# Optimization experiments

Hardware: AMD Instinct MI355X
Metric: run time of the kernel (lower is better)

The kernel has to match this reference:

```python
import jax, jax.numpy as jnp
import numpy as np

N, E, R = 50000, 800000, 8
EMB, PROJ, H, OUT = 512, 256, 256, 200


def rgcn_conv(x, src, dst, rel, W, root, bias):
    # PyG RGCNConv: per-relation linear transform, mean aggregation per relation
    # over incoming edges, summed across relations, plus root transform + bias.
    n = x.shape[0]
    r, _, out_dim = W.shape
    h = jnp.einsum('ni,rio->nro', x, W)            # [N,R,out] per-relation transforms
    msgs = h[src, rel]                             # [E,out] gather per-edge messages
    seg = dst * r + rel                            # combined (node, relation) segment id
    sums = jax.ops.segment_sum(msgs, seg, num_segments=n * r)
    cnt = jax.ops.segment_sum(jnp.ones((src.shape[0],), x.dtype), seg, num_segments=n * r)
    mean = sums / jnp.maximum(cnt, 1.0)[:, None]
    agg = mean.reshape(n, r, out_dim).sum(axis=1)  # sum over relations
    return agg + x @ root + bias


def setup_inputs() -> dict:
    key = jax.random.key(0)
    ks = jax.random.split(key, 16)
    inp = {
        'embeddings': jax.random.normal(ks[0], (N, EMB), jnp.float32),
        'node_indices': jnp.arange(N, dtype=jnp.int64) if jax.config.jax_enable_x64 else jnp.arange(N, dtype=jnp.int32),
        'src': jax.random.randint(ks[1], (E,), 0, N),
        'dst': jax.random.randint(ks[2], (E,), 0, N),
        'rel': jax.random.randint(ks[3], (E,), 0, R),
        'neg_src': jax.random.randint(ks[4], (E,), 0, N),
        'neg_dst': jax.random.randint(ks[5], (E,), 0, N),
        'neg_rel': jax.random.randint(ks[6], (E,), 0, R),
        # learned parameters
        'Wp': jax.random.normal(ks[7], (EMB, PROJ), jnp.float32) * 0.04,
        'bp': jnp.zeros((PROJ,), jnp.float32),
        'W0': jax.random.normal(ks[8], (R, PROJ, H), jnp.float32) * 0.06,
        'root0': jax.random.normal(ks[9], (PROJ, H), jnp.float32) * 0.06,
        'b0': jnp.zeros((H,), jnp.float32),
        'W1': jax.random.normal(ks[10], (R, H, H), jnp.float32) * 0.06,
        'root1': jax.random.normal(ks[11], (H, H), jnp.float32) * 0.06,
        'b1': jnp.zeros((H,), jnp.float32),
        'W2': jax.random.normal(ks[12], (R, H, OUT), jnp.float32) * 0.06,
        'root2': jax.random.normal(ks[13], (H, OUT), jnp.float32) * 0.06,
        'b2': jnp.zeros((OUT,), jnp.float32),
        'rel_emb': jax.random.normal(ks[14], (R, OUT), jnp.float32),
    }
    return inp


def reference(embeddings, node_indices, src, dst, rel, neg_src, neg_dst, neg_rel,
              Wp, bp, W0, root0, b0, W1, root1, b1, W2, root2, b2, rel_emb):
    # projection: Linear per modality, then reorder rows by node index (sort)
    proj = embeddings @ Wp + bp                        # [N,PROJ]
    x = jnp.zeros_like(proj).at[node_indices].set(proj)
    # stacked RGCN encoder with relu between layers (no relu on last)
    x = jax.nn.relu(rgcn_conv(x, src, dst, rel, W0, root0, b0))
    x = jax.nn.relu(rgcn_conv(x, src, dst, rel, W1, root1, b1))
    out = rgcn_conv(x, src, dst, rel, W2, root2, b2)   # [N,OUT]
    # DistMult decoder over positive + negative triples
    s = jnp.concatenate([src, neg_src])
    o = jnp.concatenate([dst, neg_dst])
    r = jnp.concatenate([rel, neg_rel])
    scores = jnp.sum(out[s] * rel_emb[r] * out[o], axis=-1)  # [2E]
    return out, scores
```

## Files before the change

### kernel.cpp

```cpp
#include <hip/hip_runtime.h>
#include <stdint.h>

#define NN 50000
#define NE 800000
#define NR 8
#define EMBD 512
#define PROJD 256
#define HIDD 256
#define OUTD 200
#define NSEG (NN * NR)
#define CSR_CAP 1536

typedef _Float16 half8 __attribute__((ext_vector_type(8)));
typedef _Float16 half4 __attribute__((ext_vector_type(4)));
typedef float f32x4 __attribute__((ext_vector_type(4)));

__device__ __forceinline__ void gload16(const void* g, void* l) {
    __builtin_amdgcn_global_load_lds(
        reinterpret_cast<const __attribute__((address_space(1))) uint32_t*>(
            reinterpret_cast<uintptr_t>(g)),
        reinterpret_cast<__attribute__((address_space(3))) uint32_t*>(
            reinterpret_cast<uintptr_t>(l)),
        16, 0, 0);
}


__global__ void count_edges(const int* __restrict__ dst, const int* __restrict__ rel,
                            int* __restrict__ cnt, int E) {
    int e = blockIdx.x * 256 + threadIdx.x;
    if (e >= E) return;
    atomicAdd(&cnt[dst[e] * NR + rel[e]], 1);
}

__global__ __launch_bounds__(512) void scan1(const int* __restrict__ cnt, int* __restrict__ offs,
                                             int* __restrict__ bsums, int n) {
    __shared__ int sm[512];
    int tid = threadIdx.x;
    int g = blockIdx.x * 512 + tid;
    int v = (g < n) ? cnt[g] : 0;
    sm[tid] = v;
    __syncthreads();
    for (int o = 1; o < 512; o <<= 1) {
        int t = (tid >= o) ? sm[tid - o] : 0;
        __syncthreads();
        sm[tid] += t;
        __syncthreads();
    }
    if (g < n) offs[g] = sm[tid] - v;
    if (tid == 511) bsums[blockIdx.x] = sm[511];
}

__global__ __launch_bounds__(1024) void scan2(const int* __restrict__ bsums, int* __restrict__ bpref, int nb) {
    __shared__ int sm[1024];
    int tid = threadIdx.x;
    int v = (tid < nb) ? bsums[tid] : 0;
    sm[tid] = v;
    __syncthreads();
    for (int o = 1; o < 1024; o <<= 1) {
        int t = (tid >= o) ? sm[tid - o] : 0;
        __syncthreads();
        sm[tid] += t;
        __syncthreads();
    }
    if (tid < nb) bpref[tid] = sm[tid] - v;
}

__global__ __launch_bounds__(512) void scan3(int* __restrict__ offs, int* __restrict__ cursor,
                                             const int* __restrict__ bpref, int n, int total) {
    int g = blockIdx.x * 512 + threadIdx.x;
    if (g < n) {
        int v = offs[g] + bpref[blockIdx.x];
        offs[g] = v;
        cursor[g] = v;
    }
    if (g == 0) offs[n] = total;
}

__global__ void pad_offs(int* __restrict__ offs, int total) {
    offs[NSEG + 1 + blockIdx.x * 256 + threadIdx.x] = total;
}

__global__ void scatter_edges(const int* __restrict__ dst, const int* __restrict__ rel,
                              const int* __restrict__ src, int* __restrict__ cursor,
                              int* __restrict__ csr, int E) {
    int e = blockIdx.x * 256 + threadIdx.x;
    if (e >= E) return;
    int seg = dst[e] * NR + rel[e];
    int pos = atomicAdd(&cursor[seg], 1);
    csr[pos] = src[e];
}


__global__ void f32_to_f16_vec(const float* __restrict__ in, _Float16* __restrict__ out, long n4) {
    long i = (long)blockIdx.x * 256 + threadIdx.x;
    long stride = (long)gridDim.x * 256;
    for (; i < n4; i += stride) {
        float4 v = ((const float4*)in)[i];
        half4 h;
        h[0] = (_Float16)v.x; h[1] = (_Float16)v.y; h[2] = (_Float16)v.z; h[3] = (_Float16)v.w;
        ((half4*)out)[i] = h;
    }
}

__global__ void build_bt(const float* __restrict__ S0, int K0, const float* __restrict__ S1,
                         _Float16* __restrict__ Bt, int N, int K) {
    int k = blockIdx.x * 256 + threadIdx.x;
    int n = blockIdx.y;
    if (k >= K) return;
    float v = (k < K0) ? S0[(size_t)k * N + n] : S1[(size_t)(k - K0) * N + n];
    Bt[(size_t)n * K + k] = (_Float16)v;
}


template <bool RELU, bool LAST>
__global__ __launch_bounds__(512, 4) void rgcn_layer(
    const _Float16* __restrict__ x, const _Float16* __restrict__ Bt,
    const int* __restrict__ csr, const int* __restrict__ offs,
    const float* __restrict__ bias,
    _Float16* __restrict__ C16, int ldc, float* __restrict__ C32, int N) {
    __shared__ _Float16 As[64 * 256];
    __shared__ _Float16 Bs[2][256 * 32];
    __shared__ int offs_lds[520];
    __shared__ int csr_lds[CSR_CAP];
    const int tid = threadIdx.x;
    const int lane = tid & 63, wave = tid >> 6;
    const int lane32 = tid & 31, hw = tid >> 5;
    const int half_base = lane & 32;
    const int l15 = lane & 15, q = lane >> 4;
    const int wm = wave >> 2, wn = wave & 3;
    const int m0 = blockIdx.x * 64;
    const int segbase = m0 * NR;

    for (int i = tid; i < 513; i += 512) offs_lds[i] = offs[segbase + i];
    __syncthreads();
    const int e0 = offs_lds[0];
    const int e1 = offs_lds[512];
    const int ecnt = min(e1 - e0, CSR_CAP);
    for (int i = tid; i < ecnt; i += 512) csr_lds[i] = csr[e0 + i];
    __syncthreads();

    auto stage = [&](int buf, int g) {
        int kbase = g * 32;
#pragma unroll
        for (int h = 0; h < 2; ++h) {
            int s = tid + h * 512;
            int n = s >> 2, c4 = s & 3;
            int nn = n < N ? n : N - 1;
            gload16(Bt + (size_t)nn * 2304 + kbase + ((c4 ^ (n & 3)) << 3),
                    &Bs[buf][(size_t)(wave * 64 + h * 512) * 8]);
        }
    };

    f32x4 acc[2][4] = {};
    stage(0, 0);
    int cur = 0;
    for (int seg = 0; seg < 9; ++seg) {
#pragma unroll
        for (int u = 0; u < 4; ++u) {
            int lr = u * 16 + hw;
            int nd = m0 + lr;
            if (nd >= NN) nd = NN - 1;
            half8 hv;
            if (seg == 0) {
                hv = *(const half8*)(x + (size_t)nd * 256 + lane32 * 8);
            } else {
                int sb = lr * NR + seg - 1;
                int o0 = offs_lds[sb], o1 = offs_lds[sb + 1];
                int n = o1 - o0;
                if (n < 0) n = 0;
                if (n == 0) {
#pragma unroll
                    for (int z = 0; z < 8; ++z) hv[z] = (_Float16)0.f;
                } else {
                    bool staged = (o1 - e0) <= CSR_CAP;
                    int fi = o0 + (lane32 < n ? lane32 : n - 1);
                    int idxv = staged ? csr_lds[fi - e0] : csr[fi];
                    float a0=0.f,a1=0.f,a2=0.f,a3=0.f,a4=0.f,a5=0.f,a6=0.f,a7=0.f;
                    int nb = n < 32 ? n : 32;
                    for (int e = 0; e < nb; e += 2) {
                        int s0 = __shfl(idxv, half_base + e);
                        half8 v0 = *(const half8*)(x + (size_t)s0 * 256 + lane32 * 8);
                        if (e + 1 < nb) {
                            int s1 = __shfl(idxv, half_base + e + 1);
                            half8 v1 = *(const half8*)(x + (size_t)s1 * 256 + lane32 * 8);
                            a0 += (float)v0[0] + (float)v1[0];
                            a1 += (float)v0[1] + (float)v1[1];
                            a2 += (float)v0[2] + (float)v1[2];
                            a3 += (float)v0[3] + (float)v1[3];
                            a4 += (float)v0[4] + (float)v1[4];
                            a5 += (float)v0[5] + (float)v1[5];
                            a6 += (float)v0[6] + (float)v1[6];
                            a7 += (float)v0[7] + (float)v1[7];
                        } else {
                            a0 += (float)v0[0]; a1 += (float)v0[1];
                            a2 += (float)v0[2]; a3 += (float)v0[3];
                            a4 += (float)v0[4]; a5 += (float)v0[5];
                            a6 += (float)v0[6]; a7 += (float)v0[7];
                        }
                    }
                    for (int e = 32; e < n; ++e) {
                        int s2 = staged ? csr_lds[o0 - e0 + e] : csr[o0 + e];
                        half8 v = *(const half8*)(x + (size_t)s2 * 256 + lane32 * 8);
                        a0 += (float)v[0]; a1 += (float)v[1];
                        a2 += (float)v[2]; a3 += (float)v[3];
                        a4 += (float)v[4]; a5 += (float)v[5];
                        a6 += (float)v[6]; a7 += (float)v[7];
                    }
                    float inv = 1.0f / (float)n;
                    hv[0] = (_Float16)(a0 * inv); hv[1] = (_Float16)(a1 * inv);
                    hv[2] = (_Float16)(a2 * inv); hv[3] = (_Float16)(a3 * inv);
                    hv[4] = (_Float16)(a4 * inv); hv[5] = (_Float16)(a5 * inv);
                    hv[6] = (_Float16)(a6 * inv); hv[7] = (_Float16)(a7 * inv);
                }
            }
            *(half8*)((char*)As + lr * 512 + ((lane32 ^ (lr & 31)) << 4)) = hv;
        }
        asm volatile("s_waitcnt lgkmcnt(0)" ::: "memory");
        __builtin_amdgcn_s_barrier();
        asm volatile("" ::: "memory");
        for (int ch = 0; ch < 8; ++ch) {
            int g = seg * 8 + ch;
            if (g < 71) {
                stage(cur ^ 1, g + 1);
                asm volatile("s_waitcnt vmcnt(2)" ::: "memory");
            } else {
                asm volatile("s_waitcnt vmcnt(0)" ::: "memory");
            }
            __builtin_amdgcn_s_barrier();
            asm volatile("" ::: "memory");
            half8 a[2], b[4];
#pragma unroll
            for (int i = 0; i < 2; ++i) {
                int row = wm * 32 + i * 16 + l15;
                int ck = ch * 4 + q;
                a[i] = *(const half8*)((const char*)As + row * 512 + ((ck ^ (row & 31)) << 4));
            }
#pragma unroll
            for (int j = 0; j < 4; ++j) {
                int n = wn * 64 + j * 16 + l15;
                b[j] = *(const half8*)((const char*)&Bs[cur][0] + n * 64 + ((q ^ (n & 3)) << 4));
            }
#pragma unroll
            for (int i = 0; i < 2; ++i)
#pragma unroll
                for (int j = 0; j < 4; ++j)
                    acc[i][j] = __builtin_amdgcn_mfma_f32_16x16x32_f16(a[i], b[j], acc[i][j], 0, 0, 0);
            asm volatile("s_waitcnt lgkmcnt(0)" ::: "memory");
            __builtin_amdgcn_s_barrier();
            asm volatile("" ::: "memory");
            cur ^= 1;
        }
    }
#pragma unroll
    for (int i = 0; i < 2; ++i) {
        int rbase = m0 + wm * 32 + i * 16 + q * 4;
#pragma unroll
        for (int j = 0; j < 4; ++j) {
            int cc = wn * 64 + j * 16 + l15;
            if (cc >= N) continue;
            float bv = bias[cc];
#pragma unroll
            for (int t = 0; t < 4; ++t) {
                int rr = rbase + t;
                if (rr >= NN) continue;
                float v = acc[i][j][t] + bv;
                if (RELU) v = fmaxf(v, 0.f);
                C16[(size_t)rr * ldc + cc] = (_Float16)v;
                if (LAST) C32[(size_t)rr * ldc + cc] = v;
            }
        }
    }
}


template <bool BIAS, bool ACC_IN, bool FINAL, bool RELU, bool LAST, bool SCATTER>
__global__ __launch_bounds__(256) void gemm16(
    const _Float16* __restrict__ A, int lda,
    const _Float16* __restrict__ Bt, int ldb,
    const float* __restrict__ bias, const int* __restrict__ sidx,
    _Float16* __restrict__ Cacc,
    _Float16* __restrict__ C16, int ldc, float* __restrict__ C32,
    int M, int N, int K) {
    __shared__ _Float16 As[2][4096];
    __shared__ _Float16 Bs[2][4096];
    const int tid = threadIdx.x;
    const int lane = tid & 63, wave = tid >> 6;
    const int wm = wave >> 1, wn = wave & 1;
    const int q = lane >> 4, l15 = lane & 15;
    const int m0 = blockIdx.y * 128, n0 = blockIdx.x * 128;
    const int wbase = wave * 512;
    f32x4 acc[4][4] = {};

    auto stage = [&](int buf, int k0) {
#pragma unroll
        for (int h = 0; h < 2; ++h) {
            int s = tid + h * 256;
            int r = s >> 2, c = s & 3;
            int cs = c ^ ((r >> 2) & 3);
            int ga = m0 + r; if (ga >= M) ga = M - 1;
            gload16(A + (size_t)ga * lda + k0 + cs * 8, &As[buf][wbase + h * 2048]);
            int gb = n0 + r; if (gb >= N) gb = N - 1;
            gload16(Bt + (size_t)gb * ldb + k0 + cs * 8, &Bs[buf][wbase + h * 2048]);
        }
    };

    const int nk = K >> 5;
    stage(0, 0);
    int cur = 0;
    for (int kt = 0; kt < nk; ++kt) {
        if (kt + 1 < nk) {
            stage(cur ^ 1, (kt + 1) << 5);
            asm volatile("s_waitcnt vmcnt(4)" ::: "memory");
        } else {
            asm volatile("s_waitcnt vmcnt(0)" ::: "memory");
        }
        __builtin_amdgcn_s_barrier();
        asm volatile("" ::: "memory");
        half8 a[4], b[4];
#pragma unroll
        for (int i = 0; i < 4; ++i) {
            int row = wm * 64 + i * 16 + l15;
            a[i] = *(const half8*)&As[cur][row * 32 + ((q ^ ((row >> 2) & 3)) << 3)];
            int col = wn * 64 + i * 16 + l15;
            b[i] = *(const half8*)&Bs[cur][col * 32 + ((q ^ ((col >> 2) & 3)) << 3)];
        }
#pragma unroll
        for (int i = 0; i < 4; ++i)
#pragma unroll
            for (int j = 0; j < 4; ++j)
                acc[i][j] = __builtin_amdgcn_mfma_f32_16x16x32_f16(a[i], b[j], acc[i][j], 0, 0, 0);
        asm volatile("s_waitcnt lgkmcnt(0)" ::: "memory");
        __builtin_amdgcn_s_barrier();
        asm volatile("" ::: "memory");
        cur ^= 1;
    }
#pragma unroll
    for (int i = 0; i < 4; ++i) {
        int rbase = m0 + wm * 64 + i * 16 + q * 4;
#pragma unroll
        for (int j = 0; j < 4; ++j) {
            int cc = n0 + wn * 64 + j * 16 + l15;
            if (cc >= N) continue;
#pragma unroll
            for (int t = 0; t < 4; ++t) {
                int rr = rbase + t;
                if (rr >= M) continue;
                float v = acc[i][j][t];
                if (BIAS) v += bias[cc];
                if (ACC_IN) v += (float)Cacc[(size_t)rr * 256 + cc];
                if (!FINAL) {
                    Cacc[(size_t)rr * 256 + cc] = (_Float16)v;
                } else {
                    if (RELU) v = fmaxf(v, 0.f);
                    int ro = SCATTER ? sidx[rr] : rr;
                    C16[(size_t)ro * ldc + cc] = (_Float16)v;
                    if (LAST) C32[(size_t)ro * ldc + cc] = v;
                }
            }
        }
    }
}


__global__ __launch_bounds__(256) void decoder16(
    const _Float16* __restrict__ out16, const _Float16* __restrict__ rel16,
    const int* __restrict__ src, const int* __restrict__ dst, const int* __restrict__ rel,
    const int* __restrict__ nsrc, const int* __restrict__ ndst, const int* __restrict__ nrel,
    float* __restrict__ scores) {
    int gid = blockIdx.x * 256 + threadIdx.x;
    int t = gid >> 4, lq = gid & 15;
    if (t >= 2 * NE) return;
    int s, o, r;
    if (t < NE) { s = src[t]; o = dst[t]; r = rel[t]; }
    else { int u = t - NE; s = nsrc[u]; o = ndst[u]; r = nrel[u]; }
    const half8* ps = (const half8*)(out16 + (size_t)s * OUTD);
    const half8* po = (const half8*)(out16 + (size_t)o * OUTD);
    const half8* pr = (const half8*)(rel16 + (size_t)r * OUTD);
    float acc = 0.f;
#pragma unroll
    for (int it = 0; it < 2; ++it) {
        int c = it * 16 + lq;
        if (c < 25) {
            half8 a = ps[c], b = pr[c], d = po[c];
#pragma unroll
            for (int u = 0; u < 8; ++u) acc += (float)a[u] * (float)b[u] * (float)d[u];
        }
    }
#pragma unroll
    for (int off = 8; off; off >>= 1) acc += __shfl_xor(acc, off);
    if (lq == 0) scores[t] = acc;
}


extern "C" void kernel_launch(void* const* d_in, const int* in_sizes, int n_in,
                              void* d_out, int out_size, void* d_ws, size_t ws_size,
                              hipStream_t stream) {
    const float* emb   = (const float*)d_in[0];
    const int*   nidx  = (const int*)d_in[1];
    const int*   src   = (const int*)d_in[2];
    const int*   dst   = (const int*)d_in[3];
    const int*   rel   = (const int*)d_in[4];
    const int*   nsrc  = (const int*)d_in[5];
    const int*   ndst  = (const int*)d_in[6];
    const int*   nrel  = (const int*)d_in[7];
    const float* Wp    = (const float*)d_in[8];
    const float* bp    = (const float*)d_in[9];
    const float* W0    = (const float*)d_in[10];
    const float* root0 = (const float*)d_in[11];
    const float* b0    = (const float*)d_in[12];
    const float* W1    = (const float*)d_in[13];
    const float* root1 = (const float*)d_in[14];
    const float* b1    = (const float*)d_in[15];
    const float* W2    = (const float*)d_in[16];
    const float* root2 = (const float*)d_in[17];
    const float* b2    = (const float*)d_in[18];
    const float* rele  = (const float*)d_in[19];
    (void)in_sizes; (void)n_in; (void)out_size; (void)ws_size;

    float* out    = (float*)d_out;
    float* scores = out + (size_t)NN * OUTD;

    auto align = [](size_t x) { return (x + 255) & ~(size_t)255; };
    char* p = (char*)d_ws;
    auto alloc = [&](size_t bytes) -> char* {
        char* q = p; p += align(bytes); return q;
    };
    _Float16* emb16  = (_Float16*)alloc((size_t)NN * EMBD * 2);
    _Float16* xbufA  = (_Float16*)alloc((size_t)NN * 256 * 2);
    _Float16* xbufB  = (_Float16*)alloc((size_t)NN * 256 * 2);
    _Float16* out16  = xbufB;
    _Float16* Bt0 = (_Float16*)alloc((size_t)256 * 2304 * 2);
    _Float16* Bt1 = (_Float16*)alloc((size_t)256 * 2304 * 2);
    _Float16* Bt2 = (_Float16*)alloc((size_t)256 * 2304 * 2);
    _Float16* BtP = (_Float16*)alloc((size_t)256 * EMBD * 2);
    _Float16* rel16 = (_Float16*)alloc((size_t)NR * OUTD * 2);
    int*   cnt    = (int*)alloc((size_t)NSEG * 4);
    int*   cursor = (int*)alloc((size_t)NSEG * 4);
    int*   offs   = (int*)alloc((size_t)(NSEG + 1032) * 4);
    int*   csr    = (int*)alloc((size_t)NE * 4);
    int*   bsums  = (int*)alloc(4096);
    int*   bpref  = (int*)alloc(4096);

    hipMemsetAsync(cnt, 0, (size_t)NSEG * 4, stream);
    count_edges<<<(NE + 255) / 256, 256, 0, stream>>>(dst, rel, cnt, NE);
    const int NB = (NSEG + 511) / 512;
    scan1<<<NB, 512, 0, stream>>>(cnt, offs, bsums, NSEG);
    scan2<<<1, 1024, 0, stream>>>(bsums, bpref, NB);
    scan3<<<NB, 512, 0, stream>>>(offs, cursor, bpref, NSEG, NE);
    pad_offs<<<4, 256, 0, stream>>>(offs, NE);
    scatter_edges<<<(NE + 255) / 256, 256, 0, stream>>>(dst, rel, src, cursor, csr, NE);

    f32_to_f16_vec<<<2048, 256, 0, stream>>>(emb, emb16, (long)NN * EMBD / 4);
    f32_to_f16_vec<<<2, 256, 0, stream>>>(rele, rel16, (long)NR * OUTD / 4);
    build_bt<<<dim3(2, 256), 256, 0, stream>>>(Wp, EMBD, nullptr, BtP, PROJD, EMBD);
    build_bt<<<dim3(9, 256), 256, 0, stream>>>(root0, 256, W0, Bt0, HIDD, 2304);
    build_bt<<<dim3(9, 256), 256, 0, stream>>>(root1, 256, W1, Bt1, HIDD, 2304);
    build_bt<<<dim3(9, 200), 256, 0, stream>>>(root2, 256, W2, Bt2, OUTD, 2304);

    hipMemsetAsync(xbufA, 0, (size_t)NN * 256 * 2, stream);
    {
        dim3 g(2, (NN + 127) / 128);
        gemm16<true, false, true, false, false, true><<<g, 256, 0, stream>>>(
            emb16, EMBD, BtP, EMBD, bp, nidx, nullptr, xbufA, 256, nullptr, NN, 256, EMBD);
    }

    const int GL = (NN + 63) / 64;
    rgcn_layer<true, false><<<GL, 512, 0, stream>>>(xbufA, Bt0, csr, offs, b0,
                                                    xbufB, 256, nullptr, HIDD);
    rgcn_layer<true, false><<<GL, 512, 0, stream>>>(xbufB, Bt1, csr, offs, b1,
                                                    xbufA, 256, nullptr, HIDD);
    rgcn_layer<false, true><<<GL, 512, 0, stream>>>(xbufA, Bt2, csr, offs, b2,
                                                    out16, OUTD, out, OUTD);

    decoder16<<<(2 * NE * 16 + 255) / 256, 256, 0, stream>>>(out16, rel16, src, dst, rel,
                                                             nsrc, ndst, nrel, scores);
}
```

Measured before the change: 910.5 us.

## Unroll gather by four, halve decoder lanes with fp16 math, drop memset

The neighbor-gather loop in the RGCN layer is unrolled from two to four loads per iteration so more independent global loads are in flight. The decoder now uses eight lanes per triple instead of sixteen and computes the triple product and partial sums in packed fp16, reducing in fp32 only at the end. The memset of the projection buffer is removed on the assumption that the scatter writes every row. Doing the products and accumulation in fp16 lowers precision, and dropping the memset relies on node_indices being a full permutation.

```diff
diff --git a/kernel.cpp b/kernel.cpp
--- a/kernel.cpp
+++ b/kernel.cpp
@@ -177,30 +177,36 @@
                     int idxv = staged ? csr_lds[fi - e0] : csr[fi];
                     float a0=0.f,a1=0.f,a2=0.f,a3=0.f,a4=0.f,a5=0.f,a6=0.f,a7=0.f;
                     int nb = n < 32 ? n : 32;
-                    for (int e = 0; e < nb; e += 2) {
+                    int e = 0;
+                    for (; e + 4 <= nb; e += 4) {
+                        int s0 = __shfl(idxv, half_base + e);
+                        int s1 = __shfl(idxv, half_base + e + 1);
+                        int s2 = __shfl(idxv, half_base + e + 2);
+                        int s3 = __shfl(idxv, half_base + e + 3);
+                        half8 v0 = *(const half8*)(x + (size_t)s0 * 256 + lane32 * 8);
+                        half8 v1 = *(const half8*)(x + (size_t)s1 * 256 + lane32 * 8);
+                        half8 v2 = *(const half8*)(x + (size_t)s2 * 256 + lane32 * 8);
+                        half8 v3 = *(const half8*)(x + (size_t)s3 * 256 + lane32 * 8);
+                        a0 += ((float)v0[0] + (float)v1[0]) + ((float)v2[0] + (float)v3[0]);
+                        a1 += ((float)v0[1] + (float)v1[1]) + ((float)v2[1] + (float)v3[1]);
+                        a2 += ((float)v0[2] + (float)v1[2]) + ((float)v2[2] + (float)v3[2]);
+                        a3 += ((float)v0[3] + (float)v1[3]) + ((float)v2[3] + (float)v3[3]);
+                        a4 += ((float)v0[4] + (float)v1[4]) + ((float)v2[4] + (float)v3[4]);
+                        a5 += ((float)v0[5] + (float)v1[5]) + ((float)v2[5] + (float)v3[5]);
+                        a6 += ((float)v0[6] + (float)v1[6]) + ((float)v2[6] + (float)v3[6]);
+                        a7 += ((float)v0[7] + (float)v1[7]) + ((float)v2[7] + (float)v3[7]);
+                    }
+                    for (; e < nb; ++e) {
                         int s0 = __shfl(idxv, half_base + e);
                         half8 v0 = *(const half8*)(x + (size_t)s0 * 256 + lane32 * 8);
-                        if (e + 1 < nb) {
-                            int s1 = __shfl(idxv, half_base + e + 1);
-                            half8 v1 = *(const half8*)(x + (size_t)s1 * 256 + lane32 * 8);
-                            a0 += (float)v0[0] + (float)v1[0];
-                            a1 += (float)v0[1] + (float)v1[1];
-                            a2 += (float)v0[2] + (float)v1[2];
-                            a3 += (float)v0[3] + (float)v1[3];
-                            a4 += (float)v0[4] + (float)v1[4];
-                            a5 += (float)v0[5] + (float)v1[5];
-                            a6 += (float)v0[6] + (float)v1[6];
-                            a7 += (float)v0[7] + (float)v1[7];
-                        } else {
-                            a0 += (float)v0[0]; a1 += (float)v0[1];
-                            a2 += (float)v0[2]; a3 += (float)v0[3];
-                            a4 += (float)v0[4]; a5 += (float)v0[5];
-                            a6 += (float)v0[6]; a7 += (float)v0[7];
-                        }
+                        a0 += (float)v0[0]; a1 += (float)v0[1];
+                        a2 += (float)v0[2]; a3 += (float)v0[3];
+                        a4 += (float)v0[4]; a5 += (float)v0[5];
+                        a6 += (float)v0[6]; a7 += (float)v0[7];
                     }
-                    for (int e = 32; e < n; ++e) {
-                        int s2 = staged ? csr_lds[o0 - e0 + e] : csr[o0 + e];
-                        half8 v = *(const half8*)(x + (size_t)s2 * 256 + lane32 * 8);
+                    for (int e2 = 32; e2 < n; ++e2) {
+                        int s2i = staged ? csr_lds[o0 - e0 + e2] : csr[o0 + e2];
+                        half8 v = *(const half8*)(x + (size_t)s2i * 256 + lane32 * 8);
                         a0 += (float)v[0]; a1 += (float)v[1];
                         a2 += (float)v[2]; a3 += (float)v[3];
                         a4 += (float)v[4]; a5 += (float)v[5];
@@ -368,7 +374,7 @@
     const int* __restrict__ nsrc, const int* __restrict__ ndst, const int* __restrict__ nrel,
     float* __restrict__ scores) {
     int gid = blockIdx.x * 256 + threadIdx.x;
-    int t = gid >> 4, lq = gid & 15;
+    int t = gid >> 3, lq = gid & 7;
     if (t >= 2 * NE) return;
     int s, o, r;
     if (t < NE) { s = src[t]; o = dst[t]; r = rel[t]; }
@@ -376,18 +382,21 @@
     const half8* ps = (const half8*)(out16 + (size_t)s * OUTD);
     const half8* po = (const half8*)(out16 + (size_t)o * OUTD);
     const half8* pr = (const half8*)(rel16 + (size_t)r * OUTD);
-    float acc = 0.f;
-#pragma unroll
-    for (int it = 0; it < 2; ++it) {
-        int c = it * 16 + lq;
+    half8 hacc0 = {}, hacc1 = {};
+#pragma unroll
+    for (int it = 0; it < 4; ++it) {
+        int c = it * 8 + lq;
         if (c < 25) {
             half8 a = ps[c], b = pr[c], d = po[c];
-#pragma unroll
-            for (int u = 0; u < 8; ++u) acc += (float)a[u] * (float)b[u] * (float)d[u];
-        }
-    }
-#pragma unroll
-    for (int off = 8; off; off >>= 1) acc += __shfl_xor(acc, off);
+            half8 p = a * b * d;
+            if (it & 1) hacc1 += p; else hacc0 += p;
+        }
+    }
+    float acc = 0.f;
+#pragma unroll
+    for (int u = 0; u < 8; ++u) acc += (float)hacc0[u] + (float)hacc1[u];
+#pragma unroll
+    for (int off = 4; off; off >>= 1) acc += __shfl_xor(acc, off);
     if (lq == 0) scores[t] = acc;
 }
 
@@ -457,7 +466,6 @@
     build_bt<<<dim3(9, 256), 256, 0, stream>>>(root1, 256, W1, Bt1, HIDD, 2304);
     build_bt<<<dim3(9, 200), 256, 0, stream>>>(root2, 256, W2, Bt2, OUTD, 2304);
 
-    hipMemsetAsync(xbufA, 0, (size_t)NN * 256 * 2, stream);
     {
         dim3 g(2, (NN + 127) / 128);
         gemm16<true, false, true, false, false, true><<<g, 256, 0, stream>>>(
@@ -472,6 +480,6 @@
     rgcn_layer<false, true><<<GL, 512, 0, stream>>>(xbufA, Bt2, csr, offs, b2,
                                                     out16, OUTD, out, OUTD);
 
-    decoder16<<<(2 * NE * 16 + 255) / 256, 256, 0, stream>>>(out16, rel16, src, dst, rel,
-                                                             nsrc, ndst, nrel, scores);
-}
+    decoder16<<<(2 * NE * 8 + 255) / 256, 256, 0, stream>>>(out16, rel16, src, dst, rel,
+                                                            nsrc, ndst, nrel, scores);
+}
```

New measurement: 883.0 us. 1.03x faster.
